# Performance work log

Measured on AMD Instinct MI355X. Metric: run time of the kernel, lower is better.

## Reference

```python
import jax, jax.numpy as jnp
import numpy as np


def setup_inputs() -> dict:
    key = jax.random.key(0)
    k1, k2, k3, k4 = jax.random.split(key, 4)
    N = 100000          # n_users + n_items nodes
    E = 1600000         # nonzeros in normalized adjacency (avg degree 16)
    D = 64              # embedding dim
    edge_row = jnp.sort(jax.random.randint(k1, (E,), 0, N, dtype=jnp.int32))
    edge_col = jax.random.randint(k2, (E,), 0, N, dtype=jnp.int32)
    edge_val = jax.random.uniform(k3, (E,), dtype=jnp.float32)
    embeds = jax.random.normal(k4, (N, D), dtype=jnp.float32)
    return {
        "edge_row": edge_row,
        "edge_col": edge_col,
        "edge_val": edge_val,
        "embeds": embeds,
        "num_nodes": N,
    }


def reference(edge_row, edge_col, edge_val, embeds, num_nodes):
    # out = A @ embeds, A given in COO: A[row[e], col[e]] = val[e]
    gathered = edge_val[:, None] * embeds[edge_col]        # [E, D]
    out = jax.ops.segment_sum(gathered, edge_row, num_segments=num_nodes)  # [N, D]
    return out
```

## Files before the change

### kernel.cpp

```cpp
#include <hip/hip_runtime.h>


#define GCN_D 64

typedef float f4 __attribute__((ext_vector_type(4)));

__global__ __launch_bounds__(256) void build_row_ptr_kernel(
    const int* __restrict__ edge_row, int* __restrict__ row_ptr, int E, int N)
{
    const int e = blockIdx.x * blockDim.x + threadIdx.x;
    if (e >= E) return;
    const int r    = edge_row[e];
    const int prev = (e == 0) ? -1 : edge_row[e - 1];
    for (int k = prev + 1; k <= r; ++k) row_ptr[k] = e;
    if (e == E - 1)
        for (int k = r + 1; k <= N; ++k) row_ptr[k] = E;
}

__global__ __launch_bounds__(256) void gcn_row_kernel(
    const int* __restrict__ row_ptr,
    const int* __restrict__ edge_col,
    const float* __restrict__ edge_val,
    const float* __restrict__ embeds,
    float* __restrict__ out,
    int N)
{
    const int row = (blockIdx.x * blockDim.x + threadIdx.x) >> 6;
    if (row >= N) return;
    const int lane = threadIdx.x & 63;
    const int sub  = lane >> 4;
    const int db   = (lane & 15) * 4;

    int p0 = __builtin_amdgcn_readfirstlane(row_ptr[row]);
    int p1 = __builtin_amdgcn_readfirstlane(row_ptr[row + 1]);

    f4 acc = (f4)0.0f;

    int k = p0 + sub;
    while (k + 12 < p1) {
        const int   c0 = __builtin_nontemporal_load(edge_col + k);
        const int   c1 = __builtin_nontemporal_load(edge_col + k + 4);
        const int   c2 = __builtin_nontemporal_load(edge_col + k + 8);
        const int   c3 = __builtin_nontemporal_load(edge_col + k + 12);
        const float v0 = __builtin_nontemporal_load(edge_val + k);
        const float v1 = __builtin_nontemporal_load(edge_val + k + 4);
        const float v2 = __builtin_nontemporal_load(edge_val + k + 8);
        const float v3 = __builtin_nontemporal_load(edge_val + k + 12);
        const f4 g0 = *(const f4*)(embeds + (size_t)c0 * GCN_D + db);
        const f4 g1 = *(const f4*)(embeds + (size_t)c1 * GCN_D + db);
        const f4 g2 = *(const f4*)(embeds + (size_t)c2 * GCN_D + db);
        const f4 g3 = *(const f4*)(embeds + (size_t)c3 * GCN_D + db);
        acc += v0 * g0;
        acc += v1 * g1;
        acc += v2 * g2;
        acc += v3 * g3;
        k += 16;
    }
    while (k < p1) {
        const int   c = __builtin_nontemporal_load(edge_col + k);
        const float v = __builtin_nontemporal_load(edge_val + k);
        const f4    g = *(const f4*)(embeds + (size_t)c * GCN_D + db);
        acc += v * g;
        k += 4;
    }

    acc.x += __shfl_xor(acc.x, 16); acc.y += __shfl_xor(acc.y, 16);
    acc.z += __shfl_xor(acc.z, 16); acc.w += __shfl_xor(acc.w, 16);
    acc.x += __shfl_xor(acc.x, 32); acc.y += __shfl_xor(acc.y, 32);
    acc.z += __shfl_xor(acc.z, 32); acc.w += __shfl_xor(acc.w, 32);

    if (sub == 0)
        __builtin_nontemporal_store(acc, (f4*)(out + (size_t)row * GCN_D + db));
}

extern "C" void kernel_launch(void* const* d_in, const int* in_sizes, int n_in,
                              void* d_out, int out_size, void* d_ws, size_t ws_size,
                              hipStream_t stream) {
    const int*   edge_row = (const int*)d_in[0];
    const int*   edge_col = (const int*)d_in[1];
    const float* edge_val = (const float*)d_in[2];
    const float* embeds   = (const float*)d_in[3];
    float*       out      = (float*)d_out;

    const int E = in_sizes[0];
    const int N = out_size / GCN_D;

    int* row_ptr = (int*)d_ws;

    build_row_ptr_kernel<<<(E + 255) / 256, 256, 0, stream>>>(edge_row, row_ptr, E, N);

    const int blocks = (N + 3) / 4;
    gcn_row_kernel<<<blocks, 256, 0, stream>>>(row_ptr, edge_col, edge_val,
                                               embeds, out, N);
}
```

Measured before the change: 151.8 us.

## Map one row per 16-lane group instead of per wavefront

Each row is now handled by a 16-thread group, so a 64-lane wavefront processes four rows at once. The four-way edge split inside a row and its cross-lane shuffle reduction are removed, and a plain store replaces the nontemporal one. The aim is to cut idle lanes and reduction overhead on short rows (average degree 16) and launch four times fewer waves. In exchange, the four rows in a wave can have different lengths, which causes divergence, and row_ptr and edge indices are no longer wave-uniform scalar loads.

```diff
diff --git a/kernel.cpp b/kernel.cpp
--- a/kernel.cpp
+++ b/kernel.cpp
@@ -25,27 +25,26 @@
     float* __restrict__ out,
     int N)
 {
-    const int row = (blockIdx.x * blockDim.x + threadIdx.x) >> 6;
+    const int tid = blockIdx.x * blockDim.x + threadIdx.x;
+    const int row = tid >> 4;
     if (row >= N) return;
-    const int lane = threadIdx.x & 63;
-    const int sub  = lane >> 4;
-    const int db   = (lane & 15) * 4;
+    const int db  = (threadIdx.x & 15) * 4;
 
-    int p0 = __builtin_amdgcn_readfirstlane(row_ptr[row]);
-    int p1 = __builtin_amdgcn_readfirstlane(row_ptr[row + 1]);
+    const int p0 = row_ptr[row];
+    const int p1 = row_ptr[row + 1];
 
     f4 acc = (f4)0.0f;
 
-    int k = p0 + sub;
-    while (k + 12 < p1) {
-        const int   c0 = __builtin_nontemporal_load(edge_col + k);
-        const int   c1 = __builtin_nontemporal_load(edge_col + k + 4);
-        const int   c2 = __builtin_nontemporal_load(edge_col + k + 8);
-        const int   c3 = __builtin_nontemporal_load(edge_col + k + 12);
-        const float v0 = __builtin_nontemporal_load(edge_val + k);
-        const float v1 = __builtin_nontemporal_load(edge_val + k + 4);
-        const float v2 = __builtin_nontemporal_load(edge_val + k + 8);
-        const float v3 = __builtin_nontemporal_load(edge_val + k + 12);
+    int k = p0;
+    for (; k + 3 < p1; k += 4) {
+        const int   c0 = edge_col[k];
+        const int   c1 = edge_col[k + 1];
+        const int   c2 = edge_col[k + 2];
+        const int   c3 = edge_col[k + 3];
+        const float v0 = edge_val[k];
+        const float v1 = edge_val[k + 1];
+        const float v2 = edge_val[k + 2];
+        const float v3 = edge_val[k + 3];
         const f4 g0 = *(const f4*)(embeds + (size_t)c0 * GCN_D + db);
         const f4 g1 = *(const f4*)(embeds + (size_t)c1 * GCN_D + db);
         const f4 g2 = *(const f4*)(embeds + (size_t)c2 * GCN_D + db);
@@ -54,23 +53,15 @@
         acc += v1 * g1;
         acc += v2 * g2;
         acc += v3 * g3;
-        k += 16;
     }
-    while (k < p1) {
-        const int   c = __builtin_nontemporal_load(edge_col + k);
-        const float v = __builtin_nontemporal_load(edge_val + k);
+    for (; k < p1; ++k) {
+        const int   c = edge_col[k];
+        const float v = edge_val[k];
         const f4    g = *(const f4*)(embeds + (size_t)c * GCN_D + db);
         acc += v * g;
-        k += 4;
     }
 
-    acc.x += __shfl_xor(acc.x, 16); acc.y += __shfl_xor(acc.y, 16);
-    acc.z += __shfl_xor(acc.z, 16); acc.w += __shfl_xor(acc.w, 16);
-    acc.x += __shfl_xor(acc.x, 32); acc.y += __shfl_xor(acc.y, 32);
-    acc.z += __shfl_xor(acc.z, 32); acc.w += __shfl_xor(acc.w, 32);
-
-    if (sub == 0)
-        __builtin_nontemporal_store(acc, (f4*)(out + (size_t)row * GCN_D + db));
+    *(f4*)(out + (size_t)row * GCN_D + db) = acc;
 }
 
 extern "C" void kernel_launch(void* const* d_in, const int* in_sizes, int n_in,
@@ -89,7 +80,8 @@
 
     build_row_ptr_kernel<<<(E + 255) / 256, 256, 0, stream>>>(edge_row, row_ptr, E, N);
 
-    const int blocks = (N + 3) / 4;
+    const int threads_total = N * 16;
+    const int blocks = (threads_total + 255) / 256;
     gcn_row_kernel<<<blocks, 256, 0, stream>>>(row_ptr, edge_col, edge_val,
                                                embeds, out, N);
 }
```

New measurement: 146.3 us. 1.04x faster.
